# Kernel tuning notes

Hardware: AMD Instinct MI355X
Metric: run time of the kernel (lower is better)

The kernel has to match this reference:

```python
import jax, jax.numpy as jnp
import numpy as np

N_HEADS = 16


def setup_inputs() -> dict:
    key = jax.random.key(0)
    ks = jax.random.split(key, 6)
    S, B, D = 2048, 1, 2048
    x = jax.random.normal(ks[0], (S, B, D), dtype=jnp.float32)
    qkv_weight = jax.random.normal(ks[1], (D, 3 * D), dtype=jnp.float32) * 0.02
    qkv_bias = jax.random.normal(ks[2], (3 * D,), dtype=jnp.float32) * 0.02
    attn_out_weight = jax.random.normal(ks[3], (D, D), dtype=jnp.float32) * 0.02
    attn_out_bias = jax.random.normal(ks[4], (D,), dtype=jnp.float32) * 0.02
    position_ids = jax.random.randint(ks[5], (B, 2, S), 0, S, dtype=jnp.int64 if jax.config.jax_enable_x64 else jnp.int32)
    return {"x": x, "qkv_weight": qkv_weight, "qkv_bias": qkv_bias,
            "attn_out_weight": attn_out_weight, "attn_out_bias": attn_out_bias,
            "position_ids": position_ids}


def _rope(xh, pos, inv_freq):
    # xh: [S, B, H, half], pos: [S, B], inv_freq: [half/2]
    ang = pos[..., None].astype(jnp.float32) * inv_freq          # [S, B, half/2]
    ang = jnp.concatenate([ang, ang], axis=-1)[:, :, None, :]    # [S, B, 1, half]
    x1, x2 = jnp.split(xh, 2, axis=-1)
    rot = jnp.concatenate([-x2, x1], axis=-1)                    # rotate_half
    return xh * jnp.cos(ang) + rot * jnp.sin(ang)


def reference(x, qkv_weight, qkv_bias, attn_out_weight, attn_out_bias, position_ids):
    S, B, D = x.shape
    H = N_HEADS
    hd = D // H
    half = hd // 2
    # fused QKV projection
    qkv = x @ qkv_weight + qkv_bias                              # [S, B, 3D]
    q, k, v = jnp.split(qkv, 3, axis=-1)
    q = q.reshape(S, B, H, hd)
    k = k.reshape(S, B, H, hd)
    v = v.reshape(S, B, H, hd)
    # GLM dual RoPE: two position streams, each applied to half of head_dim
    inv_freq = 1.0 / (10000.0 ** (jnp.arange(0, half, 2, dtype=jnp.float32) / half))
    pos1 = position_ids[:, 0, :].T                               # [S, B]
    pos2 = position_ids[:, 1, :].T
    q1, q2 = jnp.split(q, 2, axis=-1)
    k1, k2 = jnp.split(k, 2, axis=-1)
    q = jnp.concatenate([_rope(q1, pos1, inv_freq), _rope(q2, pos2, inv_freq)], axis=-1)
    k = jnp.concatenate([_rope(k1, pos1, inv_freq), _rope(k2, pos2, inv_freq)], axis=-1)
    # unscaled attention (original applies no 1/sqrt(head_dim) and no mask)
    logits = jnp.einsum('qbhd,kbhd->qkbh', q, k)                 # [S, S, B, H]
    probs = jax.nn.softmax(logits, axis=1)                       # softmax over key axis
    wv = jnp.einsum('qkbh,kbhd->qbhd', probs, v).reshape(S, B, D)
    return wv @ attn_out_weight + attn_out_bias
```

## Files before the change

### kernel.cpp

```cpp
#include <hip/hip_runtime.h>
#include <cmath>

typedef __attribute__((ext_vector_type(8))) _Float16 half8;
typedef __attribute__((ext_vector_type(4))) float f32x4;

#define S_LEN 2048
#define DM    2048

__device__ __forceinline__ unsigned short h2u(_Float16 h) {
    union { _Float16 h; unsigned short u; } c; c.h = h; return c.u;
}
__device__ __forceinline__ void gload16(const void* g, void* l) {
    __builtin_amdgcn_global_load_lds(
        (const __attribute__((address_space(1))) unsigned*)g,
        (__attribute__((address_space(3))) unsigned*)l, 16, 0, 0);
}

__global__ __launch_bounds__(256) void conv_x_kernel(
    const float* __restrict__ x, _Float16* __restrict__ xh)
{
    const int idx = blockIdx.x * 256 + threadIdx.x;
    const int r = idx >> 8;
    const int c = (idx & 255) << 3;
    float4 v0 = *(const float4*)(x + (size_t)r * 2048 + c);
    float4 v1 = *(const float4*)(x + (size_t)r * 2048 + c + 4);
    unsigned short o[8];
    o[0] = h2u((_Float16)v0.x); o[1] = h2u((_Float16)v0.y);
    o[2] = h2u((_Float16)v0.z); o[3] = h2u((_Float16)v0.w);
    o[4] = h2u((_Float16)v1.x); o[5] = h2u((_Float16)v1.y);
    o[6] = h2u((_Float16)v1.z); o[7] = h2u((_Float16)v1.w);
    *(uint4*)((unsigned short*)xh + (size_t)r * 2048 + c) =
        make_uint4((unsigned)o[0] | ((unsigned)o[1] << 16),
                   (unsigned)o[2] | ((unsigned)o[3] << 16),
                   (unsigned)o[4] | ((unsigned)o[5] << 16),
                   (unsigned)o[6] | ((unsigned)o[7] << 16));
}

__global__ __launch_bounds__(256) void tw_kernel(
    const float* __restrict__ W, _Float16* __restrict__ Wt, int N)
{
    __shared__ float T[64][65];
    const int t = threadIdx.x;
    const int bx = blockIdx.x;
    const int by = blockIdx.y;
    {
        const int c = (t & 15) * 4;
        const int r0 = t >> 4;
#pragma unroll
        for (int i = 0; i < 4; ++i) {
            const int r = r0 + i * 16;
            float4 v = *(const float4*)(W + (size_t)(by * 64 + r) * N + bx * 64 + c);
            T[r][c] = v.x; T[r][c + 1] = v.y; T[r][c + 2] = v.z; T[r][c + 3] = v.w;
        }
    }
    __syncthreads();
    const int n = t >> 2;
    const int kq = (t & 3) * 16;
    unsigned hp[8], lp[8];
#pragma unroll
    for (int j = 0; j < 16; j += 2) {
        float f0 = T[kq + j][n], f1 = T[kq + j + 1][n];
        _Float16 a0 = (_Float16)f0, a1 = (_Float16)f1;
        _Float16 b0 = (_Float16)(f0 - (float)a0), b1 = (_Float16)(f1 - (float)a1);
        hp[j >> 1] = (unsigned)h2u(a0) | ((unsigned)h2u(a1) << 16);
        lp[j >> 1] = (unsigned)h2u(b0) | ((unsigned)h2u(b1) << 16);
    }
    unsigned short* dst = (unsigned short*)Wt + (size_t)(bx * 64 + n) * 4096 + by * 64 + kq;
    *(uint4*)(dst)            = make_uint4(hp[0], hp[1], hp[2], hp[3]);
    *(uint4*)(dst + 8)        = make_uint4(hp[4], hp[5], hp[6], hp[7]);
    *(uint4*)(dst + 2048)     = make_uint4(lp[0], lp[1], lp[2], lp[3]);
    *(uint4*)(dst + 2048 + 8) = make_uint4(lp[4], lp[5], lp[6], lp[7]);
}

__global__ __launch_bounds__(256, 2) void gemm_split_kernel(
    const _Float16* __restrict__ A, const _Float16* __restrict__ B2t,
    const float* __restrict__ bias, float* __restrict__ C, int N, int strideA,
    int nbx, int nwg, int nbx3, int nt_lo, int nt_hi)
{
    __shared__ _Float16 As[128 * 64];
    __shared__ _Float16 Bs[128 * 64];
    const int wk = ((blockIdx.x & 7) * (nwg >> 3)) + (blockIdx.x >> 3);
    const int bx = wk % nbx, by = wk / nbx;
    const int tid = threadIdx.x;
    const int lane = tid & 63, wv = tid >> 6;
    const int lr = lane & 15, hi8 = lane >> 4, kx = lane & 7;
    const int wm = wv >> 1, wn = wv & 1;
    const int nt = (bx < nbx3) ? nt_lo : nt_hi;

    f32x4 acc[4][4];
#pragma unroll
    for (int i = 0; i < 4; ++i)
#pragma unroll
        for (int j = 0; j < 4; ++j) acc[i][j] = f32x4{0.f, 0.f, 0.f, 0.f};

    int ldso[4]; size_t goffA[4]; size_t goffB[4];
#pragma unroll
    for (int i = 0; i < 4; ++i) {
        const int gr = i * 256 + tid;
        const int rr = gr >> 3, ss = gr & 7;
        const int gg = ss ^ (rr & 7);
        ldso[i] = gr * 8;
        goffA[i] = (size_t)rr * strideA + gg * 8;
        goffB[i] = (size_t)rr * 4096 + gg * 8;
    }

    const _Float16* Abase = A + (size_t)by * 128 * strideA;
    const _Float16* Bbase = B2t + (size_t)bx * 128 * 4096;

    for (int term = 0; term < nt; ++term) {
        const _Float16* Ag = Abase;
        const _Float16* Bg = Bbase + term * 2048;
        for (int s32 = 0; s32 < 32; ++s32) {
#pragma unroll
            for (int i = 0; i < 4; ++i) gload16(Ag + goffA[i], &As[ldso[i]]);
#pragma unroll
            for (int i = 0; i < 4; ++i) gload16(Bg + goffB[i], &Bs[ldso[i]]);
            __syncthreads();
#pragma unroll
            for (int kc = 0; kc < 2; ++kc) {
                const int slot8 = ((kc * 4 + hi8) ^ kx) * 8;
                half8 aF[4], bF[4];
#pragma unroll
                for (int mt = 0; mt < 4; ++mt)
                    aF[mt] = *(const half8*)&As[(wm * 64 + mt * 16 + lr) * 64 + slot8];
#pragma unroll
                for (int nt2 = 0; nt2 < 4; ++nt2)
                    bF[nt2] = *(const half8*)&Bs[(wn * 64 + nt2 * 16 + lr) * 64 + slot8];
#pragma unroll
                for (int mt = 0; mt < 4; ++mt)
#pragma unroll
                    for (int nt2 = 0; nt2 < 4; ++nt2)
                        acc[mt][nt2] = __builtin_amdgcn_mfma_f32_16x16x32_f16(
                            aF[mt], bF[nt2], acc[mt][nt2], 0, 0, 0);
            }
            __syncthreads();
            Ag += 64; Bg += 64;
        }
    }

#pragma unroll
    for (int nt2 = 0; nt2 < 4; ++nt2) {
        const int col = bx * 128 + wn * 64 + nt2 * 16 + lr;
        const float bv = bias[col];
#pragma unroll
        for (int mt = 0; mt < 4; ++mt)
#pragma unroll
            for (int r = 0; r < 4; ++r) {
                const int row = by * 128 + wm * 64 + mt * 16 + hi8 * 4 + r;
                C[(size_t)row * N + col] = acc[mt][nt2][r] + bv;
            }
    }
}

__global__ __launch_bounds__(256) void rope_kernel(
    const float* __restrict__ qkv, const int* __restrict__ pid,
    _Float16* __restrict__ Q2, _Float16* __restrict__ K2)
{
    const int s = blockIdx.x, t = threadIdx.x;
    const int h = t >> 4, rem = t & 15, b = rem >> 3, e4 = (rem & 7) * 4;
    const size_t rb = (size_t)s * 6144;
    const int cq = h * 128 + b * 64 + e4;

    float4 q1 = *(const float4*)(qkv + rb + cq);
    float4 q2v = *(const float4*)(qkv + rb + cq + 32);
    float4 k1 = *(const float4*)(qkv + rb + 2048 + cq);
    float4 k2v = *(const float4*)(qkv + rb + 2048 + cq + 32);
    const float pos = (float)((b == 0) ? pid[s] : pid[2048 + s]);

    float qa[4] = {q1.x, q1.y, q1.z, q1.w};
    float qb[4] = {q2v.x, q2v.y, q2v.z, q2v.w};
    float ka[4] = {k1.x, k1.y, k1.z, k1.w};
    float kb[4] = {k2v.x, k2v.y, k2v.z, k2v.w};
    float qo1[4], qo2[4], ko1[4], ko2[4];
#pragma unroll
    for (int u = 0; u < 4; ++u) {
        const float j = (float)(e4 + u);
        const float invf = powf(10000.f, -j * (1.f / 32.f));
        const float ang = pos * invf;
        float sn, cs;
        sincosf(ang, &sn, &cs);
        qo1[u] = qa[u] * cs - qb[u] * sn;
        qo2[u] = qb[u] * cs + qa[u] * sn;
        ko1[u] = ka[u] * cs - kb[u] * sn;
        ko2[u] = kb[u] * cs + ka[u] * sn;
    }

    unsigned short* qd = (unsigned short*)Q2 + ((size_t)h * 2048 + s) * 128 + b * 64 + e4;
    *(ushort4*)(qd) = make_ushort4(h2u((_Float16)qo1[0]), h2u((_Float16)qo1[1]),
                                   h2u((_Float16)qo1[2]), h2u((_Float16)qo1[3]));
    *(ushort4*)(qd + 32) = make_ushort4(h2u((_Float16)qo2[0]), h2u((_Float16)qo2[1]),
                                        h2u((_Float16)qo2[2]), h2u((_Float16)qo2[3]));
    unsigned short* kd = (unsigned short*)K2 + ((size_t)h * 2048 + s) * 256 + b * 64 + e4;
    unsigned short hh[8], ll[8];
#pragma unroll
    for (int u = 0; u < 4; ++u) {
        _Float16 h1 = (_Float16)ko1[u];
        _Float16 h2v = (_Float16)ko2[u];
        hh[u] = h2u(h1);      ll[u] = h2u((_Float16)(ko1[u] - (float)h1));
        hh[4 + u] = h2u(h2v); ll[4 + u] = h2u((_Float16)(ko2[u] - (float)h2v));
    }
    *(ushort4*)(kd)       = make_ushort4(hh[0], hh[1], hh[2], hh[3]);
    *(ushort4*)(kd + 32)  = make_ushort4(hh[4], hh[5], hh[6], hh[7]);
    *(ushort4*)(kd + 128) = make_ushort4(ll[0], ll[1], ll[2], ll[3]);
    *(ushort4*)(kd + 160) = make_ushort4(ll[4], ll[5], ll[6], ll[7]);
}

__global__ __launch_bounds__(256) void tv_kernel(
    const float* __restrict__ qkv, _Float16* __restrict__ Vt)
{
    __shared__ float T[64][65];
    const int t = threadIdx.x;
    const int bs = blockIdx.x;
    const int bc = blockIdx.y;
    {
        const int c = (t & 15) * 4;
        const int r0 = t >> 4;
#pragma unroll
        for (int i = 0; i < 4; ++i) {
            const int r = r0 + i * 16;
            float4 v = *(const float4*)(qkv + (size_t)(bs * 64 + r) * 6144 + 4096 + bc * 64 + c);
            T[r][c] = v.x; T[r][c + 1] = v.y; T[r][c + 2] = v.z; T[r][c + 3] = v.w;
        }
    }
    __syncthreads();
    const int d = t >> 2;
    const int sq = (t & 3) * 16;
    const int gcol = bc * 64 + d;
    const int h = gcol >> 7, dd = gcol & 127;
    unsigned hp[8];
#pragma unroll
    for (int j = 0; j < 16; j += 2) {
        hp[j >> 1] = (unsigned)h2u((_Float16)T[sq + j][d]) |
                     ((unsigned)h2u((_Float16)T[sq + j + 1][d]) << 16);
    }
    unsigned short* dst = (unsigned short*)Vt + ((size_t)h * 128 + dd) * 2048 + bs * 64 + sq;
    *(uint4*)(dst)     = make_uint4(hp[0], hp[1], hp[2], hp[3]);
    *(uint4*)(dst + 8) = make_uint4(hp[4], hp[5], hp[6], hp[7]);
}

__global__ __launch_bounds__(256, 2) void attn_kernel(
    const _Float16* __restrict__ Q2, const _Float16* __restrict__ K2,
    const _Float16* __restrict__ Vt, _Float16* __restrict__ A2)
{
    __shared__ _Float16 Ks[64 * 256];
    __shared__ _Float16 Vs[128 * 64];
    __shared__ _Float16 Ps[4 * 16 * 72];

    const int bid = blockIdx.x;
    const int idx = bid >> 3;
    const int h = ((bid & 7) << 1) | (idx >> 5);
    const int qt = idx & 31;
    const int tid = threadIdx.x;
    const int w = tid >> 6, lane = tid & 63;
    const int lr = lane & 15, hi8 = lane >> 4, kx = lane & 7;

    half8 qf[4];
    {
        const _Float16* Qr = Q2 + ((size_t)h * 2048 + qt * 64 + w * 16 + lr) * 128;
#pragma unroll
        for (int c = 0; c < 4; ++c)
            qf[c] = *(const half8*)(Qr + c * 32 + hi8 * 8);
    }

    f32x4 acco[8];
    float mrun[4], lrun[4];
#pragma unroll
    for (int i = 0; i < 8; ++i) acco[i] = f32x4{0.f, 0.f, 0.f, 0.f};
#pragma unroll
    for (int r = 0; r < 4; ++r) { mrun[r] = -INFINITY; lrun[r] = 0.f; }

    int kl[8], kg[8];
#pragma unroll
    for (int i = 0; i < 8; ++i) {
        const int gr = i * 256 + tid;
        const int rr = gr >> 5, ss = gr & 31;
        const int gg = (ss & 24) | ((ss & 7) ^ (rr & 7));
        kl[i] = gr * 8;
        kg[i] = rr * 256 + gg * 8;
    }
    int vl[4], vg[4];
#pragma unroll
    for (int i = 0; i < 4; ++i) {
        const int gr = i * 256 + tid;
        const int rr = gr >> 3, ss = gr & 7;
        const int gg = ss ^ (rr & 7);
        vl[i] = gr * 8;
        vg[i] = rr * 2048 + gg * 8;
    }

    const _Float16* Kh = K2 + (size_t)h * 2048 * 256;
    const _Float16* Vh = Vt + (size_t)h * 128 * 2048;
    _Float16* Pw = Ps + w * 16 * 72;

    for (int kt = 0; kt < 32; ++kt) {
        {
            const _Float16* Kg = Kh + (size_t)kt * 16384;
            const _Float16* Vg = Vh + kt * 64;
#pragma unroll
            for (int i = 0; i < 8; ++i) gload16(Kg + kg[i], &Ks[kl[i]]);
#pragma unroll
            for (int i = 0; i < 4; ++i) gload16(Vg + vg[i], &Vs[vl[i]]);
        }
        __syncthreads();

        f32x4 sacc[4];
#pragma unroll
        for (int ct = 0; ct < 4; ++ct) sacc[ct] = f32x4{0.f, 0.f, 0.f, 0.f};

#pragma unroll
        for (int ct = 0; ct < 4; ++ct) {
            const int rowb = (ct * 16 + lr) * 256;
#pragma unroll
            for (int c = 0; c < 4; ++c) {
                const int g = c * 4 + hi8;
                const int slot = (g & 8) | ((g & 7) ^ kx);
                half8 kf = *(const half8*)&Ks[rowb + slot * 8];
                sacc[ct] = __builtin_amdgcn_mfma_f32_16x16x32_f16(qf[c], kf, sacc[ct], 0, 0, 0);
            }
#pragma unroll
            for (int c = 0; c < 4; ++c) {
                const int g = c * 4 + hi8;
                const int slot = 16 | (g & 8) | ((g & 7) ^ kx);
                half8 kf = *(const half8*)&Ks[rowb + slot * 8];
                sacc[ct] = __builtin_amdgcn_mfma_f32_16x16x32_f16(qf[c], kf, sacc[ct], 0, 0, 0);
            }
        }

        float scl[4];
#pragma unroll
        for (int r = 0; r < 4; ++r) {
            float tm = fmaxf(fmaxf(sacc[0][r], sacc[1][r]), fmaxf(sacc[2][r], sacc[3][r]));
            tm = fmaxf(tm, __shfl_xor(tm, 1));
            tm = fmaxf(tm, __shfl_xor(tm, 2));
            tm = fmaxf(tm, __shfl_xor(tm, 4));
            tm = fmaxf(tm, __shfl_xor(tm, 8));
            const float mnew = fmaxf(mrun[r], tm);
            const float sc = __expf(mrun[r] - mnew);
            float pv[4], ps = 0.f;
#pragma unroll
            for (int ct = 0; ct < 4; ++ct) {
                pv[ct] = __expf(sacc[ct][r] - mnew);
                ps += pv[ct];
            }
            ps += __shfl_xor(ps, 1); ps += __shfl_xor(ps, 2);
            ps += __shfl_xor(ps, 4); ps += __shfl_xor(ps, 8);
            lrun[r] = lrun[r] * sc + ps;
            mrun[r] = mnew;
            scl[r] = sc;
#pragma unroll
            for (int ct = 0; ct < 4; ++ct)
                Pw[(hi8 * 4 + r) * 72 + ct * 16 + lr] = (_Float16)pv[ct];
        }
#pragma unroll
        for (int dt = 0; dt < 8; ++dt)
#pragma unroll
            for (int r = 0; r < 4; ++r) acco[dt][r] *= scl[r];

        half8 pf0 = *(const half8*)&Pw[lr * 72 + hi8 * 8];
        half8 pf1 = *(const half8*)&Pw[lr * 72 + 32 + hi8 * 8];
#pragma unroll
        for (int dt = 0; dt < 8; ++dt) {
            const int rowb = (dt * 16 + lr) * 64;
            half8 vf0 = *(const half8*)&Vs[rowb + ((0 + hi8) ^ kx) * 8];
            half8 vf1 = *(const half8*)&Vs[rowb + ((4 + hi8) ^ kx) * 8];
            acco[dt] = __builtin_amdgcn_mfma_f32_16x16x32_f16(pf0, vf0, acco[dt], 0, 0, 0);
            acco[dt] = __builtin_amdgcn_mfma_f32_16x16x32_f16(pf1, vf1, acco[dt], 0, 0, 0);
        }
        __syncthreads();
    }

#pragma unroll
    for (int dt = 0; dt < 8; ++dt) {
        const int n = h * 128 + dt * 16 + lr;
#pragma unroll
        for (int r = 0; r < 4; ++r) {
            const int srow = qt * 64 + w * 16 + hi8 * 4 + r;
            A2[(size_t)srow * 2048 + n] = (_Float16)(acco[dt][r] / lrun[r]);
        }
    }
}

extern "C" void kernel_launch(void* const* d_in, const int* in_sizes, int n_in,
                              void* d_out, int out_size, void* d_ws, size_t ws_size,
                              hipStream_t stream)
{
    const float* x    = (const float*)d_in[0];
    const float* Wqkv = (const float*)d_in[1];
    const float* bqkv = (const float*)d_in[2];
    const float* Wo   = (const float*)d_in[3];
    const float* bo   = (const float*)d_in[4];
    const int*   pid  = (const int*)d_in[5];
    float* out = (float*)d_out;
    char* ws = (char*)d_ws;

    const size_t MB = 1u << 20;
    _Float16* xh   = (_Float16*)(ws);
    _Float16* Wq2t = (_Float16*)(ws + 16 * MB);
    float*    qkv  = (float*)(ws + 64 * MB);
    _Float16* Q2   = (_Float16*)(ws + 16 * MB);
    _Float16* K2   = (_Float16*)(ws + 32 * MB);
    _Float16* Vtb  = (_Float16*)(ws + 48 * MB);
    _Float16* Wo2t = (_Float16*)(ws);
    _Float16* A2   = (_Float16*)(ws + 56 * MB);

    conv_x_kernel<<<2048, 256, 0, stream>>>(x, xh);
    tw_kernel<<<dim3(96, 32), 256, 0, stream>>>(Wqkv, Wq2t, 6144);
    gemm_split_kernel<<<768, 256, 0, stream>>>(xh, Wq2t, bqkv, qkv, 6144, 2048, 48, 768, 32, 2, 1);
    rope_kernel<<<2048, 256, 0, stream>>>(qkv, pid, Q2, K2);
    tv_kernel<<<dim3(32, 32), 256, 0, stream>>>(qkv, Vtb);
    tw_kernel<<<dim3(32, 32), 256, 0, stream>>>(Wo, Wo2t, 2048);

    attn_kernel<<<512, 256, 0, stream>>>(Q2, K2, Vtb, A2);

    gemm_split_kernel<<<256, 256, 0, stream>>>(A2, Wo2t, bo, out, 2048, 2048, 16, 256, 16, 2, 2);
}
```

Baseline: 406.6 us.

## Fuse split-GEMM terms into one K loop and transpose attention score layout

The split-precision GEMM now loads the A tile once per K step and applies it to both the hi and lo B halves, using a second LDS buffer, instead of re-streaming A for each term. This halves A traffic and barrier count for two-term tiles, at the cost of extra LDS per block that may lower occupancy. The attention kernel swaps the MFMA operand order so each lane holds one query row. The softmax max/sum reductions then need only two cross-lane shuffles instead of four per row, and P is written to LDS in packed pairs.

```diff
diff --git a/kernel.cpp b/kernel.cpp
--- a/kernel.cpp
+++ b/kernel.cpp
@@ -79,6 +79,7 @@
 {
     __shared__ _Float16 As[128 * 64];
     __shared__ _Float16 Bs[128 * 64];
+    __shared__ _Float16 Bs2[128 * 64];
     const int wk = ((blockIdx.x & 7) * (nwg >> 3)) + (blockIdx.x >> 3);
     const int bx = wk % nbx, by = wk / nbx;
     const int tid = threadIdx.x;
@@ -104,28 +105,39 @@
         goffB[i] = (size_t)rr * 4096 + gg * 8;
     }
 
-    const _Float16* Abase = A + (size_t)by * 128 * strideA;
-    const _Float16* Bbase = B2t + (size_t)bx * 128 * 4096;
-
-    for (int term = 0; term < nt; ++term) {
-        const _Float16* Ag = Abase;
-        const _Float16* Bg = Bbase + term * 2048;
-        for (int s32 = 0; s32 < 32; ++s32) {
-#pragma unroll
-            for (int i = 0; i < 4; ++i) gload16(Ag + goffA[i], &As[ldso[i]]);
-#pragma unroll
-            for (int i = 0; i < 4; ++i) gload16(Bg + goffB[i], &Bs[ldso[i]]);
-            __syncthreads();
-#pragma unroll
-            for (int kc = 0; kc < 2; ++kc) {
-                const int slot8 = ((kc * 4 + hi8) ^ kx) * 8;
-                half8 aF[4], bF[4];
-#pragma unroll
-                for (int mt = 0; mt < 4; ++mt)
-                    aF[mt] = *(const half8*)&As[(wm * 64 + mt * 16 + lr) * 64 + slot8];
+    const _Float16* Ag = A + (size_t)by * 128 * strideA;
+    const _Float16* Bg = B2t + (size_t)bx * 128 * 4096;
+
+    for (int s32 = 0; s32 < 32; ++s32) {
+#pragma unroll
+        for (int i = 0; i < 4; ++i) gload16(Ag + goffA[i], &As[ldso[i]]);
+#pragma unroll
+        for (int i = 0; i < 4; ++i) gload16(Bg + goffB[i], &Bs[ldso[i]]);
+        if (nt == 2) {
+#pragma unroll
+            for (int i = 0; i < 4; ++i) gload16(Bg + 2048 + goffB[i], &Bs2[ldso[i]]);
+        }
+        __syncthreads();
+#pragma unroll
+        for (int kc = 0; kc < 2; ++kc) {
+            const int slot8 = ((kc * 4 + hi8) ^ kx) * 8;
+            half8 aF[4], bF[4];
+#pragma unroll
+            for (int mt = 0; mt < 4; ++mt)
+                aF[mt] = *(const half8*)&As[(wm * 64 + mt * 16 + lr) * 64 + slot8];
+#pragma unroll
+            for (int nt2 = 0; nt2 < 4; ++nt2)
+                bF[nt2] = *(const half8*)&Bs[(wn * 64 + nt2 * 16 + lr) * 64 + slot8];
+#pragma unroll
+            for (int mt = 0; mt < 4; ++mt)
 #pragma unroll
                 for (int nt2 = 0; nt2 < 4; ++nt2)
-                    bF[nt2] = *(const half8*)&Bs[(wn * 64 + nt2 * 16 + lr) * 64 + slot8];
+                    acc[mt][nt2] = __builtin_amdgcn_mfma_f32_16x16x32_f16(
+                        aF[mt], bF[nt2], acc[mt][nt2], 0, 0, 0);
+            if (nt == 2) {
+#pragma unroll
+                for (int nt2 = 0; nt2 < 4; ++nt2)
+                    bF[nt2] = *(const half8*)&Bs2[(wn * 64 + nt2 * 16 + lr) * 64 + slot8];
 #pragma unroll
                 for (int mt = 0; mt < 4; ++mt)
 #pragma unroll
@@ -133,9 +145,9 @@
                         acc[mt][nt2] = __builtin_amdgcn_mfma_f32_16x16x32_f16(
                             aF[mt], bF[nt2], acc[mt][nt2], 0, 0, 0);
             }
-            __syncthreads();
-            Ag += 64; Bg += 64;
-        }
+        }
+        __syncthreads();
+        Ag += 64; Bg += 64;
     }
 
 #pragma unroll
@@ -263,11 +275,9 @@
     }
 
     f32x4 acco[8];
-    float mrun[4], lrun[4];
+    float mrun = -INFINITY, lrun = 0.f;
 #pragma unroll
     for (int i = 0; i < 8; ++i) acco[i] = f32x4{0.f, 0.f, 0.f, 0.f};
-#pragma unroll
-    for (int r = 0; r < 4; ++r) { mrun[r] = -INFINITY; lrun[r] = 0.f; }
 
     int kl[8], kg[8];
 #pragma unroll
@@ -315,46 +325,63 @@
                 const int g = c * 4 + hi8;
                 const int slot = (g & 8) | ((g & 7) ^ kx);
                 half8 kf = *(const half8*)&Ks[rowb + slot * 8];
-                sacc[ct] = __builtin_amdgcn_mfma_f32_16x16x32_f16(qf[c], kf, sacc[ct], 0, 0, 0);
+                sacc[ct] = __builtin_amdgcn_mfma_f32_16x16x32_f16(kf, qf[c], sacc[ct], 0, 0, 0);
             }
 #pragma unroll
             for (int c = 0; c < 4; ++c) {
                 const int g = c * 4 + hi8;
                 const int slot = 16 | (g & 8) | ((g & 7) ^ kx);
                 half8 kf = *(const half8*)&Ks[rowb + slot * 8];
-                sacc[ct] = __builtin_amdgcn_mfma_f32_16x16x32_f16(qf[c], kf, sacc[ct], 0, 0, 0);
+                sacc[ct] = __builtin_amdgcn_mfma_f32_16x16x32_f16(kf, qf[c], sacc[ct], 0, 0, 0);
             }
         }
 
-        float scl[4];
-#pragma unroll
-        for (int r = 0; r < 4; ++r) {
-            float tm = fmaxf(fmaxf(sacc[0][r], sacc[1][r]), fmaxf(sacc[2][r], sacc[3][r]));
-            tm = fmaxf(tm, __shfl_xor(tm, 1));
-            tm = fmaxf(tm, __shfl_xor(tm, 2));
-            tm = fmaxf(tm, __shfl_xor(tm, 4));
-            tm = fmaxf(tm, __shfl_xor(tm, 8));
-            const float mnew = fmaxf(mrun[r], tm);
-            const float sc = __expf(mrun[r] - mnew);
-            float pv[4], ps = 0.f;
-#pragma unroll
-            for (int ct = 0; ct < 4; ++ct) {
-                pv[ct] = __expf(sacc[ct][r] - mnew);
-                ps += pv[ct];
+        float tm;
+        {
+            float t0 = fmaxf(fmaxf(sacc[0][0], sacc[0][1]), fmaxf(sacc[0][2], sacc[0][3]));
+            float t1 = fmaxf(fmaxf(sacc[1][0], sacc[1][1]), fmaxf(sacc[1][2], sacc[1][3]));
+            float t2 = fmaxf(fmaxf(sacc[2][0], sacc[2][1]), fmaxf(sacc[2][2], sacc[2][3]));
+            float t3 = fmaxf(fmaxf(sacc[3][0], sacc[3][1]), fmaxf(sacc[3][2], sacc[3][3]));
+            tm = fmaxf(fmaxf(t0, t1), fmaxf(t2, t3));
+        }
+        tm = fmaxf(tm, __shfl_xor(tm, 16));
+        tm = fmaxf(tm, __shfl_xor(tm, 32));
+        const float mnew = fmaxf(mrun, tm);
+        const float sc = __expf(mrun - mnew);
+        float p[4][4];
+        float ps = 0.f;
+#pragma unroll
+        for (int ct = 0; ct < 4; ++ct) {
+            float s0 = __expf(sacc[ct][0] - mnew);
+            float s1 = __expf(sacc[ct][1] - mnew);
+            float s2 = __expf(sacc[ct][2] - mnew);
+            float s3 = __expf(sacc[ct][3] - mnew);
+            p[ct][0] = s0; p[ct][1] = s1; p[ct][2] = s2; p[ct][3] = s3;
+            ps += (s0 + s1) + (s2 + s3);
+        }
+        ps += __shfl_xor(ps, 16);
+        ps += __shfl_xor(ps, 32);
+        lrun = lrun * sc + ps;
+        mrun = mnew;
+
+#pragma unroll
+        for (int ct = 0; ct < 4; ++ct) {
+#pragma unroll
+            for (int hh = 0; hh < 2; ++hh) {
+                union { _Float16 h[2]; unsigned u; } pk;
+                pk.h[0] = (_Float16)p[ct][2 * hh];
+                pk.h[1] = (_Float16)p[ct][2 * hh + 1];
+                *(unsigned*)&Pw[lr * 72 + ct * 16 + hi8 * 4 + 2 * hh] = pk.u;
             }
-            ps += __shfl_xor(ps, 1); ps += __shfl_xor(ps, 2);
-            ps += __shfl_xor(ps, 4); ps += __shfl_xor(ps, 8);
-            lrun[r] = lrun[r] * sc + ps;
-            mrun[r] = mnew;
-            scl[r] = sc;
-#pragma unroll
-            for (int ct = 0; ct < 4; ++ct)
-                Pw[(hi8 * 4 + r) * 72 + ct * 16 + lr] = (_Float16)pv[ct];
-        }
+        }
+
+        float sc4[4];
+#pragma unroll
+        for (int r = 0; r < 4; ++r) sc4[r] = __shfl(sc, hi8 * 4 + r);
 #pragma unroll
         for (int dt = 0; dt < 8; ++dt)
 #pragma unroll
-            for (int r = 0; r < 4; ++r) acco[dt][r] *= scl[r];
+            for (int r = 0; r < 4; ++r) acco[dt][r] *= sc4[r];
 
         half8 pf0 = *(const half8*)&Pw[lr * 72 + hi8 * 8];
         half8 pf1 = *(const half8*)&Pw[lr * 72 + 32 + hi8 * 8];
@@ -369,13 +396,16 @@
         __syncthreads();
     }
 
+    float inv4[4];
+#pragma unroll
+    for (int r = 0; r < 4; ++r) inv4[r] = 1.f / __shfl(lrun, hi8 * 4 + r);
 #pragma unroll
     for (int dt = 0; dt < 8; ++dt) {
         const int n = h * 128 + dt * 16 + lr;
 #pragma unroll
         for (int r = 0; r < 4; ++r) {
             const int srow = qt * 64 + w * 16 + hi8 * 4 + r;
-            A2[(size_t)srow * 2048 + n] = (_Float16)(acco[dt][r] / lrun[r]);
+            A2[(size_t)srow * 2048 + n] = (_Float16)(acco[dt][r] * inv4[r]);
         }
     }
 }
```

Measured after the change: 372.5 us. 8.4% less time.
